# Kernel tuning notes

Measured on AMD Instinct MI355X. Metric: run time of the kernel, lower is better.

Reference implementation:

```python
import jax, jax.numpy as jnp
import numpy as np

N = 50000      # nodes
E = 1600000    # edges
H = 128        # node_hidden_size
T = 2          # num_prop_rounds


def setup_inputs() -> dict:
    key = jax.random.key(0)
    ks = jax.random.split(key, 10)
    s = 0.05
    return {
        "hv": jax.random.normal(ks[0], (N, H), dtype=jnp.float32),
        "edge_src": jax.random.randint(ks[1], (E,), 0, N, dtype=jnp.int64)
            if jax.config.jax_enable_x64 else jax.random.randint(ks[1], (E,), 0, N, dtype=jnp.int32),
        "edge_dst": jax.random.randint(ks[2], (E,), 0, N, dtype=jnp.int32),
        "msg_W": jax.random.normal(ks[3], (T, 2 * H, 2 * H), dtype=jnp.float32) * s,
        "msg_b": jax.random.normal(ks[4], (T, 2 * H), dtype=jnp.float32) * s,
        "gru_Wih": jax.random.normal(ks[5], (T, 3 * H, 2 * H), dtype=jnp.float32) * s,
        "gru_Whh": jax.random.normal(ks[6], (T, 3 * H, H), dtype=jnp.float32) * s,
        "gru_bih": jax.random.normal(ks[7], (T, 3 * H), dtype=jnp.float32) * s,
        "gru_bhh": jax.random.normal(ks[8], (T, 3 * H), dtype=jnp.float32) * s,
    }


def _gru_cell(a, h, Wih, Whh, bih, bhh):
    # PyTorch GRUCell gate order: reset, update, new
    gi = a @ Wih.T + bih           # [N, 3H]
    gh = h @ Whh.T + bhh           # [N, 3H]
    i_r, i_z, i_n = jnp.split(gi, 3, axis=-1)
    h_r, h_z, h_n = jnp.split(gh, 3, axis=-1)
    r = jax.nn.sigmoid(i_r + h_r)
    z = jax.nn.sigmoid(i_z + h_z)
    n = jnp.tanh(i_n + r * h_n)
    return (1.0 - z) * n + z * h


def reference(hv, edge_src, edge_dst, msg_W, msg_b, gru_Wih, gru_Whh, gru_bih, gru_bhh):
    n_nodes = hv.shape[0]
    for t in range(msg_W.shape[0]):
        # per-edge message: Linear(concat([h_dst, h_src]))  -> [E, 2H]
        h_src = hv[edge_src]
        h_dst = hv[edge_dst]
        msg = jnp.concatenate([h_dst, h_src], axis=-1) @ msg_W[t].T + msg_b[t]
        # mailbox sum per destination node -> activation a [N, 2H]
        a = jax.ops.segment_sum(msg, edge_dst, num_segments=n_nodes)
        # GRU update
        hv = _gru_cell(a, hv, gru_Wih[t], gru_Whh[t], gru_bih[t], gru_bhh[t])
    return hv
```

## Files before the change

kernel.cpp:

```cpp
#include <hip/hip_runtime.h>
#include <hip/hip_bf16.h>


#define NN 50000
#define NE 1600000
#define HH 128
#define TT 2
#define NB 1563
#define GG 64
#define EPB 25000
#define MAXB 3072

typedef _Float16 half8 __attribute__((ext_vector_type(8)));
typedef _Float16 half2v __attribute__((ext_vector_type(2)));
typedef float floatx4 __attribute__((ext_vector_type(4)));

__device__ __forceinline__ float bf2f(unsigned short u) {
    union { unsigned int i; float f; } c;
    c.i = ((unsigned int)u) << 16;
    return c.f;
}
__device__ __forceinline__ float ldf(const void* p, size_t i, int f32) {
    return f32 ? ((const float*)p)[i] : bf2f(((const unsigned short*)p)[i]);
}

__global__ void detect_kernel(const unsigned short* __restrict__ hv_u16,
                              const int* __restrict__ src, int* __restrict__ flags) {
    int i = threadIdx.x;
    int garbage = 0;
    for (int k = 0; k < 4; k++) {
        unsigned short u = hv_u16[2 * (i * 4 + k)];
        int e = (u >> 7) & 0xFF;
        if (e >= 0x90 || (e <= 0x60 && (u & 0x7FFF) != 0)) garbage++;
    }
    unsigned long long gb = __ballot(garbage > 0);
    int odd = src[2 * i + 1];
    unsigned long long bal = __ballot(odd == 0);
    if (i == 0) {
        flags[1] = (__popcll(gb) >= 8) ? 1 : 0;
        flags[0] = (bal == 0xFFFFFFFFFFFFFFFFull) ? 1 : 0;
    }
}

__global__ void split_kernel(const void* __restrict__ in, _Float16* __restrict__ ph,
                             _Float16* __restrict__ pl, int n, const int* __restrict__ flags) {
    int i = blockIdx.x * blockDim.x + threadIdx.x;
    if (i >= n) return;
    float v = ldf(in, i, flags[1]);
    _Float16 h = (_Float16)v;
    ph[i] = h;
    pl[i] = (_Float16)(v - (float)h);
}

__global__ void conv3_kernel(
    const void* __restrict__ i1, float* __restrict__ o1, int n1,
    const void* __restrict__ i2, float* __restrict__ o2, int n2,
    const void* __restrict__ i3, float* __restrict__ o3, int n3,
    const int* __restrict__ flags) {
    int i = blockIdx.x * blockDim.x + threadIdx.x;
    const void* in; float* out; int j = i;
    if (j < n1) { in = i1; out = o1; }
    else { j -= n1;
        if (j < n2) { in = i2; out = o2; }
        else { j -= n2; if (j >= n3) return; in = i3; out = o3; }
    }
    out[j] = ldf(in, j, flags[1]);
}

__global__ __launch_bounds__(256) void wc_kernel(
    const void* __restrict__ gWih, const void* __restrict__ msgW,
    _Float16* __restrict__ wcH, _Float16* __restrict__ wcL,
    const int* __restrict__ flags) {
    __shared__ float wrow[256];
    int tr = blockIdx.x;
    int t = tr / 384;
    int k = threadIdx.x;
    int f32 = flags[1];
    wrow[k] = ldf(gWih, (size_t)tr * 256 + k, f32);
    __syncthreads();
    float s = 0.f;
    size_t base = (size_t)t * 256 * 256;
    for (int c = 0; c < 256; c++)
        s += wrow[c] * ldf(msgW, base + (size_t)c * 256 + k, f32);
    _Float16 h = (_Float16)s;
    wcH[(size_t)tr * 256 + k] = h;
    wcL[(size_t)tr * 256 + k] = (_Float16)(s - (float)h);
}

__global__ void c1_kernel(const void* __restrict__ gWih, const float* __restrict__ bMsg,
                          float* __restrict__ c1, const int* __restrict__ flags) {
    int tr = blockIdx.x * 64 + threadIdx.x;
    if (tr >= TT * 384) return;
    int t = tr / 384;
    int f32 = flags[1];
    float s = 0.f;
    for (int c = 0; c < 256; c++)
        s += ldf(gWih, (size_t)tr * 256 + c, f32) * bMsg[t * 256 + c];
    c1[tr] = s;
}

__global__ __launch_bounds__(256) void bucket_hist_kernel(const int* __restrict__ dst,
                                                          int* __restrict__ counts ) {
    __shared__ int h[NB];
    int g = blockIdx.x, tid = threadIdx.x;
    for (int b = tid; b < NB; b += 256) h[b] = 0;
    __syncthreads();
    int beg = g * EPB, end = min(NE, beg + EPB);
    for (int e = beg + tid; e < end; e += 256) atomicAdd(&h[dst[e] >> 5], 1);
    __syncthreads();
    for (int b = tid; b < NB; b += 256) counts[b * GG + g] = h[b];
}

__global__ __launch_bounds__(256) void bucket_sum_kernel(const int* __restrict__ counts,
                                                         int* __restrict__ bsum) {
    int b = blockIdx.x * 4 + (threadIdx.x >> 6);
    int lane = threadIdx.x & 63;
    if (b >= NB) return;
    int v = counts[b * GG + lane];
    #pragma unroll
    for (int off = 32; off > 0; off >>= 1) v += __shfl_down(v, off, 64);
    if (lane == 0) bsum[b] = v;
}

__global__ void bucket_scan_kernel(const int* __restrict__ bsum, int* __restrict__ bbase) {
    __shared__ int wsum[16];
    __shared__ int s_running;
    int tid = threadIdx.x, lane = tid & 63, w = tid >> 6;
    if (tid == 0) s_running = 0;
    __syncthreads();
    int nch = (NB + 1024) / 1024;
    for (int c = 0; c < nch; c++) {
        int idx = c * 1024 + tid;
        int v = (idx < NB) ? bsum[idx] : 0;
        int s = v;
        #pragma unroll
        for (int off = 1; off < 64; off <<= 1) {
            int t = __shfl_up(s, off, 64);
            if (lane >= off) s += t;
        }
        if (lane == 63) wsum[w] = s;
        __syncthreads();
        if (w == 0) {
            int ws = (lane < 16) ? wsum[lane] : 0;
            #pragma unroll
            for (int off = 1; off < 16; off <<= 1) {
                int t = __shfl_up(ws, off, 64);
                if (lane >= off) ws += t;
            }
            if (lane < 16) wsum[lane] = ws;
        }
        __syncthreads();
        int incl = s + ((w > 0) ? wsum[w - 1] : 0);
        int base = s_running;
        if (idx <= NB) bbase[idx] = base + incl - v;
        __syncthreads();
        if (tid == 1023) s_running = base + incl;
        __syncthreads();
    }
}

__global__ __launch_bounds__(256) void bucket_offsets_kernel(const int* __restrict__ counts,
                                                             const int* __restrict__ bbase,
                                                             int* __restrict__ offsets) {
    int b = blockIdx.x * 4 + (threadIdx.x >> 6);
    int lane = threadIdx.x & 63;
    if (b >= NB) return;
    int v = counts[b * GG + lane];
    int s = v;
    #pragma unroll
    for (int off = 1; off < 64; off <<= 1) {
        int t = __shfl_up(s, off, 64);
        if (lane >= off) s += t;
    }
    offsets[b * GG + lane] = bbase[b] + s - v;
}

__global__ __launch_bounds__(256) void bucket_scatter_kernel(
    const int* __restrict__ src, const int* __restrict__ dst,
    const int* __restrict__ offsets, int* __restrict__ pairs,
    const int* __restrict__ flags) {
    __shared__ int ofs[NB];
    int g = blockIdx.x, tid = threadIdx.x;
    for (int b = tid; b < NB; b += 256) ofs[b] = offsets[b * GG + g];
    __syncthreads();
    int beg = g * EPB, end = min(NE, beg + EPB);
    int f64 = flags[0];
    for (int e = beg + tid; e < end; e += 256) {
        int d = dst[e];
        int s = f64 ? src[2 * e] : src[e];
        int pos = atomicAdd(&ofs[d >> 5], 1);
        pairs[pos] = ((d & 31) << 16) | s;
    }
}

__global__ __launch_bounds__(256) void bucket_sort_kernel(
    const int* __restrict__ bbase, int* __restrict__ pairs,
    int* __restrict__ row, int* __restrict__ deg) {
    __shared__ int buf[MAXB];
    __shared__ int cnt[32];
    __shared__ int off[32];
    int b = blockIdx.x, tid = threadIdx.x;
    int beg = bbase[b], end = bbase[b + 1];
    int nE = end - beg;
    if (nE > MAXB) nE = MAXB;
    if (tid < 32) cnt[tid] = 0;
    __syncthreads();
    for (int i = tid; i < nE; i += 256) {
        int pk = pairs[beg + i];
        buf[i] = pk;
        atomicAdd(&cnt[pk >> 16], 1);
    }
    __syncthreads();
    if (tid < 64) {
        int lane = tid;
        int v = (lane < 32) ? cnt[lane] : 0;
        int s = v;
        #pragma unroll
        for (int o = 1; o < 32; o <<= 1) {
            int t = __shfl_up(s, o, 64);
            if (lane >= o) s += t;
        }
        if (lane < 32) {
            off[lane] = s - v;
            int gn = b * 32 + lane;
            if (gn < NN) { row[gn] = beg + s - v; deg[gn] = v; }
        }
        if (lane == 0 && b == NB - 1) row[NN] = end;
    }
    __syncthreads();
    if (tid < 32) cnt[tid] = off[tid];
    __syncthreads();
    for (int i = tid; i < nE; i += 256) {
        int pk = buf[i];
        int pos = atomicAdd(&cnt[pk >> 16], 1);
        pairs[beg + pos] = pk & 0xFFFF;
    }
}

__global__ __launch_bounds__(64) void gather_kernel(
    const int* __restrict__ row, const int* __restrict__ csr,
    const _Float16* __restrict__ hvH,
    _Float16* __restrict__ SH, _Float16* __restrict__ SL) {
    int n = blockIdx.x;
    int lane = threadIdx.x;
    const half2v* hv2 = (const half2v*)hvH;
    int beg = row[n], end = row[n + 1];
    float sx = 0.f, sy = 0.f;
    int e = beg;
    for (; e + 8 <= end; e += 8) {
        int s0 = csr[e], s1 = csr[e + 1], s2 = csr[e + 2], s3 = csr[e + 3];
        int s4 = csr[e + 4], s5 = csr[e + 5], s6 = csr[e + 6], s7 = csr[e + 7];
        half2v v0 = hv2[(size_t)s0 * 64 + lane];
        half2v v1 = hv2[(size_t)s1 * 64 + lane];
        half2v v2 = hv2[(size_t)s2 * 64 + lane];
        half2v v3 = hv2[(size_t)s3 * 64 + lane];
        half2v v4 = hv2[(size_t)s4 * 64 + lane];
        half2v v5 = hv2[(size_t)s5 * 64 + lane];
        half2v v6 = hv2[(size_t)s6 * 64 + lane];
        half2v v7 = hv2[(size_t)s7 * 64 + lane];
        sx += (float)v0.x + (float)v1.x + (float)v2.x + (float)v3.x
            + (float)v4.x + (float)v5.x + (float)v6.x + (float)v7.x;
        sy += (float)v0.y + (float)v1.y + (float)v2.y + (float)v3.y
            + (float)v4.y + (float)v5.y + (float)v6.y + (float)v7.y;
    }
    for (; e < end; e++) {
        half2v v = hv2[(size_t)csr[e] * 64 + lane];
        sx += (float)v.x; sy += (float)v.y;
    }
    half2v hx, lx;
    hx.x = (_Float16)sx; lx.x = (_Float16)(sx - (float)hx.x);
    hx.y = (_Float16)sy; lx.y = (_Float16)(sy - (float)hx.y);
    ((half2v*)SH)[(size_t)n * 64 + lane] = hx;
    ((half2v*)SL)[(size_t)n * 64 + lane] = lx;
}

struct GemmOp {
    const _Float16 *AhA, *AlA, *AhB, *AlB;
    int Kleft, K;
    const _Float16 *Wh, *Wl;
    const float* bias;
    const float* bias2;
    _Float16* outH;
    int ldc, mode;
};

__global__ __launch_bounds__(256) void mfma_gemm_kernel(
    GemmOp op, const int* __restrict__ deg, int M) {
    __shared__ _Float16 Wsh[128][40];
    __shared__ _Float16 Wsl[128][40];
    int n0 = blockIdx.x * 128;
    int m0 = blockIdx.y * 128;
    int tid = threadIdx.x;
    int wave = tid >> 6, lane = tid & 63;
    int lr = lane & 15, quad = lane >> 4;
    int wm = wave * 32;
    floatx4 acc[2][8] = {};
    int r0 = tid >> 2, c0 = (tid & 3) * 8;

    float dsc[2] = {1.f, 1.f};
    if (op.mode == 0) {
        #pragma unroll
        for (int mt = 0; mt < 2; mt++) {
            int gm = m0 + wm + mt * 16 + lr;
            dsc[mt] = (gm < M) ? (float)deg[gm] : 0.f;
        }
    }

    for (int k0 = 0; k0 < op.K; k0 += 32) {
        half8 wh0 = *(const half8*)(op.Wh + (size_t)(n0 + r0) * op.K + k0 + c0);
        half8 wh1 = *(const half8*)(op.Wh + (size_t)(n0 + r0 + 64) * op.K + k0 + c0);
        half8 wl0 = *(const half8*)(op.Wl + (size_t)(n0 + r0) * op.K + k0 + c0);
        half8 wl1 = *(const half8*)(op.Wl + (size_t)(n0 + r0 + 64) * op.K + k0 + c0);
        bool left = (k0 < op.Kleft);
        const _Float16* Ph = left ? op.AhA : op.AhB;
        const _Float16* Pl = left ? op.AlA : op.AlB;
        int astr = left ? op.Kleft : (op.K - op.Kleft);
        int kk = (left ? k0 : k0 - op.Kleft) + quad * 8;
        half8 afh[2] = {}, afl[2] = {};
        #pragma unroll
        for (int mt = 0; mt < 2; mt++) {
            int gm = m0 + wm + mt * 16 + lr;
            if (gm < M) {
                afh[mt] = *(const half8*)(Ph + (size_t)gm * astr + kk);
                afl[mt] = *(const half8*)(Pl + (size_t)gm * astr + kk);
            }
        }
        if (op.mode == 0 && left) {
            #pragma unroll
            for (int mt = 0; mt < 2; mt++)
                #pragma unroll
                for (int q = 0; q < 8; q++) {
                    float f = ((float)afh[mt][q] + (float)afl[mt][q]) * dsc[mt];
                    _Float16 h = (_Float16)f;
                    afh[mt][q] = h; afl[mt][q] = (_Float16)(f - (float)h);
                }
        }
        __syncthreads();
        *(half8*)&Wsh[r0][c0] = wh0;   *(half8*)&Wsh[r0 + 64][c0] = wh1;
        *(half8*)&Wsl[r0][c0] = wl0;   *(half8*)&Wsl[r0 + 64][c0] = wl1;
        __syncthreads();
        #pragma unroll
        for (int nt = 0; nt < 8; nt++) {
            half8 bh = *(const half8*)&Wsh[nt * 16 + lr][quad * 8];
            half8 bl = *(const half8*)&Wsl[nt * 16 + lr][quad * 8];
            #pragma unroll
            for (int mt = 0; mt < 2; mt++) {
                acc[mt][nt] = __builtin_amdgcn_mfma_f32_16x16x32_f16(afh[mt], bh, acc[mt][nt], 0, 0, 0);
                acc[mt][nt] = __builtin_amdgcn_mfma_f32_16x16x32_f16(afl[mt], bh, acc[mt][nt], 0, 0, 0);
                acc[mt][nt] = __builtin_amdgcn_mfma_f32_16x16x32_f16(afh[mt], bl, acc[mt][nt], 0, 0, 0);
            }
        }
    }

    #pragma unroll
    for (int mt = 0; mt < 2; mt++) {
        #pragma unroll
        for (int r = 0; r < 4; r++) {
            int m = m0 + wm + mt * 16 + quad * 4 + r;
            if (m >= M) continue;
            float d2 = (op.mode == 0) ? (float)deg[m] : 0.f;
            #pragma unroll
            for (int nt = 0; nt < 8; nt++) {
                int n = n0 + nt * 16 + lr;
                float v = acc[mt][nt][r] + op.bias[n];
                if (op.mode == 0) v += d2 * op.bias2[n];
                op.outH[(size_t)m * op.ldc + n] = (_Float16)v;
            }
        }
    }
}

__global__ void gate_kernel(const _Float16* __restrict__ gi,
                            const _Float16* __restrict__ gh,
                            _Float16* __restrict__ hvH, _Float16* __restrict__ hvL,
                            void* __restrict__ outv,
                            const int* __restrict__ flags, int writeOut, int total) {
    int idx = blockIdx.x * blockDim.x + threadIdx.x;
    if (idx >= total) return;
    int n = idx >> 7;
    int j = idx & 127;
    size_t base = (size_t)n * 384;
    float i_r = (float)gi[base + j];
    float i_z = (float)gi[base + 128 + j];
    float i_n = (float)gi[base + 256 + j];
    float h_r = (float)gh[base + j];
    float h_z = (float)gh[base + 128 + j];
    float h_n = (float)gh[base + 256 + j];
    float h = (float)hvH[idx] + (float)hvL[idx];
    float r = 1.f / (1.f + __expf(-(i_r + h_r)));
    float z = 1.f / (1.f + __expf(-(i_z + h_z)));
    float nn = tanhf(i_n + r * h_n);
    float hn = (1.f - z) * nn + z * h;
    _Float16 hh = (_Float16)hn;
    hvH[idx] = hh;
    hvL[idx] = (_Float16)(hn - (float)hh);
    if (writeOut) {
        if (flags[1]) ((float*)outv)[idx] = hn;
        else ((__hip_bfloat16*)outv)[idx] = __float2bfloat16(hn);
    }
}

extern "C" void kernel_launch(void* const* d_in, const int* in_sizes, int n_in,
                              void* d_out, int out_size, void* d_ws, size_t ws_size,
                              hipStream_t stream) {
    const void* hv_in   = d_in[0];
    const int* edge_src = (const int*)d_in[1];
    const int* edge_dst = (const int*)d_in[2];
    const void* msg_W = d_in[3];
    const void* msg_b = d_in[4];
    const void* gWih  = d_in[5];
    const void* gWhh  = d_in[6];
    const void* gbih  = d_in[7];
    const void* gbhh  = d_in[8];

    char* p = (char*)d_ws;
    auto alloc = [&](size_t bytes) -> void* {
        void* r = (void*)p;
        p += (bytes + 255) & ~(size_t)255;
        return r;
    };
    int* flags   = (int*)alloc(256);
    int* deg     = (int*)alloc((size_t)NN * 4);
    int* row     = (int*)alloc((size_t)(NN + 1) * 4);
    int* counts  = (int*)alloc((size_t)NB * GG * 4);
    int* bsum    = (int*)alloc((size_t)NB * 4);
    int* bbase   = (int*)alloc((size_t)(NB + 1) * 4);
    int* offsets = (int*)alloc((size_t)NB * GG * 4);
    int* pairs   = (int*)alloc((size_t)NE * 4);
    _Float16* wCcH = (_Float16*)alloc((size_t)TT * 384 * 256 * 2);
    _Float16* wCcL = (_Float16*)alloc((size_t)TT * 384 * 256 * 2);
    _Float16* wHhH = (_Float16*)alloc((size_t)TT * 384 * 128 * 2);
    _Float16* wHhL = (_Float16*)alloc((size_t)TT * 384 * 128 * 2);
    float* bMsg = (float*)alloc((size_t)TT * 256 * 4);
    float* bIh  = (float*)alloc((size_t)TT * 384 * 4);
    float* bHh  = (float*)alloc((size_t)TT * 384 * 4);
    float* c1   = (float*)alloc((size_t)TT * 384 * 4);
    _Float16* hvH = (_Float16*)alloc((size_t)NN * HH * 2);
    _Float16* hvL = (_Float16*)alloc((size_t)NN * HH * 2);
    char* PA = (char*)alloc((size_t)NN * 384 * 2);
    char* PB = (char*)alloc((size_t)NN * 384 * 2);
    (void)ws_size; (void)in_sizes; (void)n_in; (void)out_size;

    _Float16* gi = (_Float16*)PA;
    _Float16* SH = (_Float16*)PB;
    _Float16* SL = (_Float16*)(PB + (size_t)NN * HH * 2);
    _Float16* gh = (_Float16*)PB;

    detect_kernel<<<1, 64, 0, stream>>>((const unsigned short*)hv_in, edge_src, flags);
    split_kernel<<<(NN * HH + 255) / 256, 256, 0, stream>>>(hv_in, hvH, hvL, NN * HH, flags);
    split_kernel<<<(TT * 384 * 128 + 255) / 256, 256, 0, stream>>>(
        gWhh, wHhH, wHhL, TT * 384 * 128, flags);
    {
        int n1 = TT * 256, n2 = TT * 384, n3 = TT * 384;
        conv3_kernel<<<(n1 + n2 + n3 + 255) / 256, 256, 0, stream>>>(
            msg_b, bMsg, n1, gbih, bIh, n2, gbhh, bHh, n3, flags);
    }
    wc_kernel<<<TT * 384, 256, 0, stream>>>(gWih, msg_W, wCcH, wCcL, flags);
    c1_kernel<<<(TT * 384 + 63) / 64, 64, 0, stream>>>(gWih, bMsg, c1, flags);

    bucket_hist_kernel<<<GG, 256, 0, stream>>>(edge_dst, counts);
    bucket_sum_kernel<<<(NB + 3) / 4, 256, 0, stream>>>(counts, bsum);
    bucket_scan_kernel<<<1, 1024, 0, stream>>>(bsum, bbase);
    bucket_offsets_kernel<<<(NB + 3) / 4, 256, 0, stream>>>(counts, bbase, offsets);
    bucket_scatter_kernel<<<GG, 256, 0, stream>>>(edge_src, edge_dst, offsets, pairs, flags);
    bucket_sort_kernel<<<NB, 256, 0, stream>>>(bbase, pairs, row, deg);

    int mt128 = (NN + 127) / 128;

    for (int t = 0; t < TT; t++) {
        gather_kernel<<<NN, 64, 0, stream>>>(row, pairs, hvH, SH, SL);

        GemmOp opi = { hvH, hvL, SH, SL, 128, 256,
                       wCcH + (size_t)t * 384 * 256, wCcL + (size_t)t * 384 * 256,
                       bIh + (size_t)t * 384, c1 + (size_t)t * 384, gi, 384, 0 };
        mfma_gemm_kernel<<<dim3(3, mt128), 256, 0, stream>>>(opi, deg, NN);

        GemmOp opg = { hvH, hvL, hvH, hvL, 128, 128,
                       wHhH + (size_t)t * 384 * 128, wHhL + (size_t)t * 384 * 128,
                       bHh + (size_t)t * 384, nullptr, gh, 384, 1 };
        mfma_gemm_kernel<<<dim3(3, mt128), 256, 0, stream>>>(opg, deg, NN);

        gate_kernel<<<(NN * HH + 255) / 256, 256, 0, stream>>>(
            gi, gh, hvH, hvL, d_out, flags, (t == TT - 1) ? 1 : 0, NN * HH);
    }
}
```

Measured before the change: 595.2 us.

## Fuse both GRU GEMMs and the gate into one per-round kernel

Replaces the two MFMA GEMM launches (input-side and hidden-side) and the separate gate kernel with a single fused kernel per round. Each 64-thread block handles 32 rows and 64 output columns, and computes the r, z and n gate chunks in turn, keeping r and z in shared memory. The last chunk applies the GRU update directly. This removes the global round-trip of the gi/gh intermediates (N x 384 fp16 each) and two launches, and double-buffers the hidden state so the kernel does not read rows it has already overwritten. In exchange, weights are now read straight from global memory with no shared-memory staging. The tiles are also small single-wave blocks, which may lower MFMA efficiency and increase weight traffic.

```diff
diff --git a/kernel.cpp b/kernel.cpp
--- a/kernel.cpp
+++ b/kernel.cpp
@@ -274,129 +274,140 @@
     ((half2v*)SL)[(size_t)n * 64 + lane] = lx;
 }
 
-struct GemmOp {
-    const _Float16 *AhA, *AlA, *AhB, *AlB;
-    int Kleft, K;
-    const _Float16 *Wh, *Wl;
-    const float* bias;
-    const float* bias2;
-    _Float16* outH;
-    int ldc, mode;
-};
-
-__global__ __launch_bounds__(256) void mfma_gemm_kernel(
-    GemmOp op, const int* __restrict__ deg, int M) {
-    __shared__ _Float16 Wsh[128][40];
-    __shared__ _Float16 Wsl[128][40];
-    int n0 = blockIdx.x * 128;
-    int m0 = blockIdx.y * 128;
-    int tid = threadIdx.x;
-    int wave = tid >> 6, lane = tid & 63;
-    int lr = lane & 15, quad = lane >> 4;
-    int wm = wave * 32;
-    floatx4 acc[2][8] = {};
-    int r0 = tid >> 2, c0 = (tid & 3) * 8;
-
-    float dsc[2] = {1.f, 1.f};
-    if (op.mode == 0) {
-        #pragma unroll
-        for (int mt = 0; mt < 2; mt++) {
-            int gm = m0 + wm + mt * 16 + lr;
-            dsc[mt] = (gm < M) ? (float)deg[gm] : 0.f;
-        }
-    }
-
-    for (int k0 = 0; k0 < op.K; k0 += 32) {
-        half8 wh0 = *(const half8*)(op.Wh + (size_t)(n0 + r0) * op.K + k0 + c0);
-        half8 wh1 = *(const half8*)(op.Wh + (size_t)(n0 + r0 + 64) * op.K + k0 + c0);
-        half8 wl0 = *(const half8*)(op.Wl + (size_t)(n0 + r0) * op.K + k0 + c0);
-        half8 wl1 = *(const half8*)(op.Wl + (size_t)(n0 + r0 + 64) * op.K + k0 + c0);
-        bool left = (k0 < op.Kleft);
-        const _Float16* Ph = left ? op.AhA : op.AhB;
-        const _Float16* Pl = left ? op.AlA : op.AlB;
-        int astr = left ? op.Kleft : (op.K - op.Kleft);
-        int kk = (left ? k0 : k0 - op.Kleft) + quad * 8;
-        half8 afh[2] = {}, afl[2] = {};
-        #pragma unroll
-        for (int mt = 0; mt < 2; mt++) {
-            int gm = m0 + wm + mt * 16 + lr;
-            if (gm < M) {
-                afh[mt] = *(const half8*)(Ph + (size_t)gm * astr + kk);
-                afl[mt] = *(const half8*)(Pl + (size_t)gm * astr + kk);
-            }
-        }
-        if (op.mode == 0 && left) {
+__global__ __launch_bounds__(64) void fused_round_kernel(
+    const _Float16* __restrict__ hvH, const _Float16* __restrict__ hvL,
+    const _Float16* __restrict__ SH, const _Float16* __restrict__ SL,
+    const _Float16* __restrict__ WcH, const _Float16* __restrict__ WcL,
+    const _Float16* __restrict__ WhH, const _Float16* __restrict__ WhL,
+    const float* __restrict__ bIh, const float* __restrict__ bHh,
+    const float* __restrict__ c1v, const int* __restrict__ deg,
+    _Float16* __restrict__ newH, _Float16* __restrict__ newL,
+    void* __restrict__ outv, const int* __restrict__ flags, int writeOut) {
+    __shared__ _Float16 rbuf[32][72];
+    __shared__ _Float16 zbuf[32][72];
+    const int cg = blockIdx.x;
+    const int m0 = blockIdx.y * 32;
+    const int lane = threadIdx.x;
+    const int lr = lane & 15, quad = lane >> 4;
+    const int kq = quad * 8;
+
+    int gmA[2]; bool vA[2];
+    #pragma unroll
+    for (int mt = 0; mt < 2; mt++) { gmA[mt] = m0 + mt * 16 + lr; vA[mt] = gmA[mt] < NN; }
+
+    float dmr[2][4];
+    #pragma unroll
+    for (int mt = 0; mt < 2; mt++)
+        #pragma unroll
+        for (int r = 0; r < 4; r++) {
+            int om = m0 + mt * 16 + quad * 4 + r;
+            dmr[mt][r] = (om < NN) ? (float)deg[om] : 0.f;
+        }
+
+    #pragma clang loop unroll(disable)
+    for (int c = 0; c < 3; c++) {
+        const int nb = c * 128 + cg * 64;
+        floatx4 accR[2][4], accL[2][4], accH[2][4];
+        #pragma unroll
+        for (int nt = 0; nt < 4; nt++) {
+            int n = nb + nt * 16 + lr;
+            float bi = bIh[n], cc = c1v[n], bg = bHh[n];
             #pragma unroll
             for (int mt = 0; mt < 2; mt++)
                 #pragma unroll
-                for (int q = 0; q < 8; q++) {
-                    float f = ((float)afh[mt][q] + (float)afl[mt][q]) * dsc[mt];
-                    _Float16 h = (_Float16)f;
-                    afh[mt][q] = h; afl[mt][q] = (_Float16)(f - (float)h);
+                for (int q = 0; q < 4; q++) {
+                    accR[mt][nt][q] = bi;
+                    accL[mt][nt][q] = cc;
+                    accH[mt][nt][q] = bg;
                 }
         }
-        __syncthreads();
-        *(half8*)&Wsh[r0][c0] = wh0;   *(half8*)&Wsh[r0 + 64][c0] = wh1;
-        *(half8*)&Wsl[r0][c0] = wl0;   *(half8*)&Wsl[r0 + 64][c0] = wl1;
-        __syncthreads();
-        #pragma unroll
-        for (int nt = 0; nt < 8; nt++) {
-            half8 bh = *(const half8*)&Wsh[nt * 16 + lr][quad * 8];
-            half8 bl = *(const half8*)&Wsl[nt * 16 + lr][quad * 8];
-            #pragma unroll
-            for (int mt = 0; mt < 2; mt++) {
-                acc[mt][nt] = __builtin_amdgcn_mfma_f32_16x16x32_f16(afh[mt], bh, acc[mt][nt], 0, 0, 0);
-                acc[mt][nt] = __builtin_amdgcn_mfma_f32_16x16x32_f16(afl[mt], bh, acc[mt][nt], 0, 0, 0);
-                acc[mt][nt] = __builtin_amdgcn_mfma_f32_16x16x32_f16(afh[mt], bl, acc[mt][nt], 0, 0, 0);
-            }
-        }
-    }
-
-    #pragma unroll
-    for (int mt = 0; mt < 2; mt++) {
-        #pragma unroll
-        for (int r = 0; r < 4; r++) {
-            int m = m0 + wm + mt * 16 + quad * 4 + r;
-            if (m >= M) continue;
-            float d2 = (op.mode == 0) ? (float)deg[m] : 0.f;
-            #pragma unroll
-            for (int nt = 0; nt < 8; nt++) {
-                int n = n0 + nt * 16 + lr;
-                float v = acc[mt][nt][r] + op.bias[n];
-                if (op.mode == 0) v += d2 * op.bias2[n];
-                op.outH[(size_t)m * op.ldc + n] = (_Float16)v;
-            }
-        }
-    }
-}
-
-__global__ void gate_kernel(const _Float16* __restrict__ gi,
-                            const _Float16* __restrict__ gh,
-                            _Float16* __restrict__ hvH, _Float16* __restrict__ hvL,
-                            void* __restrict__ outv,
-                            const int* __restrict__ flags, int writeOut, int total) {
-    int idx = blockIdx.x * blockDim.x + threadIdx.x;
-    if (idx >= total) return;
-    int n = idx >> 7;
-    int j = idx & 127;
-    size_t base = (size_t)n * 384;
-    float i_r = (float)gi[base + j];
-    float i_z = (float)gi[base + 128 + j];
-    float i_n = (float)gi[base + 256 + j];
-    float h_r = (float)gh[base + j];
-    float h_z = (float)gh[base + 128 + j];
-    float h_n = (float)gh[base + 256 + j];
-    float h = (float)hvH[idx] + (float)hvL[idx];
-    float r = 1.f / (1.f + __expf(-(i_r + h_r)));
-    float z = 1.f / (1.f + __expf(-(i_z + h_z)));
-    float nn = tanhf(i_n + r * h_n);
-    float hn = (1.f - z) * nn + z * h;
-    _Float16 hh = (_Float16)hn;
-    hvH[idx] = hh;
-    hvL[idx] = (_Float16)(hn - (float)hh);
-    if (writeOut) {
-        if (flags[1]) ((float*)outv)[idx] = hn;
-        else ((__hip_bfloat16*)outv)[idx] = __float2bfloat16(hn);
+        #pragma unroll
+        for (int k0 = 0; k0 < 128; k0 += 32) {
+            half8 afh[2] = {}, afl[2] = {};
+            #pragma unroll
+            for (int mt = 0; mt < 2; mt++) if (vA[mt]) {
+                afh[mt] = *(const half8*)(SH + (size_t)gmA[mt] * HH + k0 + kq);
+                afl[mt] = *(const half8*)(SL + (size_t)gmA[mt] * HH + k0 + kq);
+            }
+            #pragma unroll
+            for (int nt = 0; nt < 4; nt++) {
+                size_t wi = (size_t)(nb + nt * 16 + lr) * 256 + 128 + k0 + kq;
+                half8 bh = *(const half8*)(WcH + wi);
+                half8 bl = *(const half8*)(WcL + wi);
+                #pragma unroll
+                for (int mt = 0; mt < 2; mt++) {
+                    accR[mt][nt] = __builtin_amdgcn_mfma_f32_16x16x32_f16(afh[mt], bh, accR[mt][nt], 0, 0, 0);
+                    accR[mt][nt] = __builtin_amdgcn_mfma_f32_16x16x32_f16(afl[mt], bh, accR[mt][nt], 0, 0, 0);
+                    accR[mt][nt] = __builtin_amdgcn_mfma_f32_16x16x32_f16(afh[mt], bl, accR[mt][nt], 0, 0, 0);
+                }
+            }
+        }
+        #pragma unroll
+        for (int k0 = 0; k0 < 128; k0 += 32) {
+            half8 afh[2] = {}, afl[2] = {};
+            #pragma unroll
+            for (int mt = 0; mt < 2; mt++) if (vA[mt]) {
+                afh[mt] = *(const half8*)(hvH + (size_t)gmA[mt] * HH + k0 + kq);
+                afl[mt] = *(const half8*)(hvL + (size_t)gmA[mt] * HH + k0 + kq);
+            }
+            #pragma unroll
+            for (int nt = 0; nt < 4; nt++) {
+                size_t wi = (size_t)(nb + nt * 16 + lr) * 256 + k0 + kq;
+                half8 bh = *(const half8*)(WcH + wi);
+                half8 bl = *(const half8*)(WcL + wi);
+                #pragma unroll
+                for (int mt = 0; mt < 2; mt++) {
+                    accL[mt][nt] = __builtin_amdgcn_mfma_f32_16x16x32_f16(afh[mt], bh, accL[mt][nt], 0, 0, 0);
+                    accL[mt][nt] = __builtin_amdgcn_mfma_f32_16x16x32_f16(afl[mt], bh, accL[mt][nt], 0, 0, 0);
+                    accL[mt][nt] = __builtin_amdgcn_mfma_f32_16x16x32_f16(afh[mt], bl, accL[mt][nt], 0, 0, 0);
+                }
+            }
+            #pragma unroll
+            for (int nt = 0; nt < 4; nt++) {
+                size_t wi = (size_t)(nb + nt * 16 + lr) * HH + k0 + kq;
+                half8 bh = *(const half8*)(WhH + wi);
+                half8 bl = *(const half8*)(WhL + wi);
+                #pragma unroll
+                for (int mt = 0; mt < 2; mt++) {
+                    accH[mt][nt] = __builtin_amdgcn_mfma_f32_16x16x32_f16(afh[mt], bh, accH[mt][nt], 0, 0, 0);
+                    accH[mt][nt] = __builtin_amdgcn_mfma_f32_16x16x32_f16(afl[mt], bh, accH[mt][nt], 0, 0, 0);
+                    accH[mt][nt] = __builtin_amdgcn_mfma_f32_16x16x32_f16(afh[mt], bl, accH[mt][nt], 0, 0, 0);
+                }
+            }
+        }
+        #pragma unroll
+        for (int mt = 0; mt < 2; mt++)
+            #pragma unroll
+            for (int nt = 0; nt < 4; nt++)
+                #pragma unroll
+                for (int r = 0; r < 4; r++) {
+                    int lrow = mt * 16 + quad * 4 + r;
+                    int lcol = nt * 16 + lr;
+                    float gi = dmr[mt][r] * accL[mt][nt][r] + accR[mt][nt][r];
+                    float gh = accH[mt][nt][r];
+                    if (c == 0) {
+                        rbuf[lrow][lcol] = (_Float16)(1.f / (1.f + __expf(-(gi + gh))));
+                    } else if (c == 1) {
+                        zbuf[lrow][lcol] = (_Float16)(1.f / (1.f + __expf(-(gi + gh))));
+                    } else {
+                        int om = m0 + lrow;
+                        if (om < NN) {
+                            float rv = (float)rbuf[lrow][lcol];
+                            float zv = (float)zbuf[lrow][lcol];
+                            float nv = tanhf(gi + rv * gh);
+                            size_t hidx = (size_t)om * HH + cg * 64 + lcol;
+                            float h = (float)hvH[hidx] + (float)hvL[hidx];
+                            float hn = (1.f - zv) * nv + zv * h;
+                            _Float16 hh = (_Float16)hn;
+                            newH[hidx] = hh;
+                            newL[hidx] = (_Float16)(hn - (float)hh);
+                            if (writeOut) {
+                                if (flags[1]) ((float*)outv)[hidx] = hn;
+                                else ((__hip_bfloat16*)outv)[hidx] = __float2bfloat16(hn);
+                            }
+                        }
+                    }
+                }
     }
 }
 
@@ -435,19 +446,16 @@
     float* bIh  = (float*)alloc((size_t)TT * 384 * 4);
     float* bHh  = (float*)alloc((size_t)TT * 384 * 4);
     float* c1   = (float*)alloc((size_t)TT * 384 * 4);
-    _Float16* hvH = (_Float16*)alloc((size_t)NN * HH * 2);
-    _Float16* hvL = (_Float16*)alloc((size_t)NN * HH * 2);
-    char* PA = (char*)alloc((size_t)NN * 384 * 2);
-    char* PB = (char*)alloc((size_t)NN * 384 * 2);
+    _Float16* hvAH = (_Float16*)alloc((size_t)NN * HH * 2);
+    _Float16* hvAL = (_Float16*)alloc((size_t)NN * HH * 2);
+    _Float16* hvBH = (_Float16*)alloc((size_t)NN * HH * 2);
+    _Float16* hvBL = (_Float16*)alloc((size_t)NN * HH * 2);
+    _Float16* SH   = (_Float16*)alloc((size_t)NN * HH * 2);
+    _Float16* SL   = (_Float16*)alloc((size_t)NN * HH * 2);
     (void)ws_size; (void)in_sizes; (void)n_in; (void)out_size;
 
-    _Float16* gi = (_Float16*)PA;
-    _Float16* SH = (_Float16*)PB;
-    _Float16* SL = (_Float16*)(PB + (size_t)NN * HH * 2);
-    _Float16* gh = (_Float16*)PB;
-
     detect_kernel<<<1, 64, 0, stream>>>((const unsigned short*)hv_in, edge_src, flags);
-    split_kernel<<<(NN * HH + 255) / 256, 256, 0, stream>>>(hv_in, hvH, hvL, NN * HH, flags);
+    split_kernel<<<(NN * HH + 255) / 256, 256, 0, stream>>>(hv_in, hvAH, hvAL, NN * HH, flags);
     split_kernel<<<(TT * 384 * 128 + 255) / 256, 256, 0, stream>>>(
         gWhh, wHhH, wHhL, TT * 384 * 128, flags);
     {
@@ -465,22 +473,21 @@
     bucket_scatter_kernel<<<GG, 256, 0, stream>>>(edge_src, edge_dst, offsets, pairs, flags);
     bucket_sort_kernel<<<NB, 256, 0, stream>>>(bbase, pairs, row, deg);
 
-    int mt128 = (NN + 127) / 128;
+    const int mt32 = (NN + 31) / 32;
+    _Float16 *cH = hvAH, *cL = hvAL, *nH = hvBH, *nL = hvBL;
 
     for (int t = 0; t < TT; t++) {
-        gather_kernel<<<NN, 64, 0, stream>>>(row, pairs, hvH, SH, SL);
-
-        GemmOp opi = { hvH, hvL, SH, SL, 128, 256,
-                       wCcH + (size_t)t * 384 * 256, wCcL + (size_t)t * 384 * 256,
-                       bIh + (size_t)t * 384, c1 + (size_t)t * 384, gi, 384, 0 };
-        mfma_gemm_kernel<<<dim3(3, mt128), 256, 0, stream>>>(opi, deg, NN);
-
-        GemmOp opg = { hvH, hvL, hvH, hvL, 128, 128,
-                       wHhH + (size_t)t * 384 * 128, wHhL + (size_t)t * 384 * 128,
-                       bHh + (size_t)t * 384, nullptr, gh, 384, 1 };
-        mfma_gemm_kernel<<<dim3(3, mt128), 256, 0, stream>>>(opg, deg, NN);
-
-        gate_kernel<<<(NN * HH + 255) / 256, 256, 0, stream>>>(
-            gi, gh, hvH, hvL, d_out, flags, (t == TT - 1) ? 1 : 0, NN * HH);
-    }
-}
+        gather_kernel<<<NN, 64, 0, stream>>>(row, pairs, cH, SH, SL);
+
+        fused_round_kernel<<<dim3(2, mt32), 64, 0, stream>>>(
+            cH, cL, SH, SL,
+            wCcH + (size_t)t * 384 * 256, wCcL + (size_t)t * 384 * 256,
+            wHhH + (size_t)t * 384 * 128, wHhL + (size_t)t * 384 * 128,
+            bIh + (size_t)t * 384, bHh + (size_t)t * 384, c1 + (size_t)t * 384,
+            deg, nH, nL, d_out, flags, (t == TT - 1) ? 1 : 0);
+
+        _Float16* sw;
+        sw = cH; cH = nH; nH = sw;
+        sw = cL; cL = nL; nL = sw;
+    }
+}
```

Measured after the change: 838.6 us. 40.9% more time.

## Template GEMM with whole-K weight tile in LDS, XCD-aware block remap

Applied to the files above, without the earlier changes.

Replaces the runtime-parameterized GEMM with a templated kernel that loads the full-K weight slice for a 64-column tile into shared memory once, so the K loop no longer has per-step barriers. The degree scaling of the hv-part is moved out of the per-element split/recombine and applied in the epilogue through a separate left accumulator. Block IDs are remapped so neighbouring tiles land on the same XCD, and the grid becomes 1D with 64-wide N tiles. In exchange it doubles A-matrix reloads across N tiles and uses more LDS per block.

```diff
diff --git a/kernel.cpp b/kernel.cpp
--- a/kernel.cpp
+++ b/kernel.cpp
@@ -274,80 +274,93 @@
     ((half2v*)SL)[(size_t)n * 64 + lane] = lx;
 }
 
-struct GemmOp {
-    const _Float16 *AhA, *AlA, *AhB, *AlB;
-    int Kleft, K;
-    const _Float16 *Wh, *Wl;
-    const float* bias;
-    const float* bias2;
-    _Float16* outH;
-    int ldc, mode;
-};
-
-__global__ __launch_bounds__(256) void mfma_gemm_kernel(
-    GemmOp op, const int* __restrict__ deg, int M) {
-    __shared__ _Float16 Wsh[128][40];
-    __shared__ _Float16 Wsl[128][40];
-    int n0 = blockIdx.x * 128;
-    int m0 = blockIdx.y * 128;
+template<int KK, int KLEFT, int MODE>
+__global__ __launch_bounds__(256) void gemm_t(
+    const _Float16* __restrict__ AhA, const _Float16* __restrict__ AlA,
+    const _Float16* __restrict__ AhB, const _Float16* __restrict__ AlB,
+    const _Float16* __restrict__ Wh,  const _Float16* __restrict__ Wl,
+    const float* __restrict__ bias, const float* __restrict__ bias2,
+    _Float16* __restrict__ outC, const int* __restrict__ deg, int M) {
+    constexpr int LDW = KK + 8;
+    __shared__ _Float16 Wsh[64][LDW];
+    __shared__ _Float16 Wsl[64][LDW];
+
+    int nwg = gridDim.x;
+    int q = nwg >> 3, r = nwg & 7;
+    int xcd = blockIdx.x & 7, pos = blockIdx.x >> 3;
+    int wid = (xcd < r ? xcd * (q + 1) : r * (q + 1) + (xcd - r) * q) + pos;
+    int n0 = (wid % 6) * 64;
+    int m0 = (wid / 6) * 128;
+
     int tid = threadIdx.x;
     int wave = tid >> 6, lane = tid & 63;
     int lr = lane & 15, quad = lane >> 4;
     int wm = wave * 32;
-    floatx4 acc[2][8] = {};
-    int r0 = tid >> 2, c0 = (tid & 3) * 8;
-
-    float dsc[2] = {1.f, 1.f};
-    if (op.mode == 0) {
-        #pragma unroll
-        for (int mt = 0; mt < 2; mt++) {
-            int gm = m0 + wm + mt * 16 + lr;
-            dsc[mt] = (gm < M) ? (float)deg[gm] : 0.f;
-        }
-    }
-
-    for (int k0 = 0; k0 < op.K; k0 += 32) {
-        half8 wh0 = *(const half8*)(op.Wh + (size_t)(n0 + r0) * op.K + k0 + c0);
-        half8 wh1 = *(const half8*)(op.Wh + (size_t)(n0 + r0 + 64) * op.K + k0 + c0);
-        half8 wl0 = *(const half8*)(op.Wl + (size_t)(n0 + r0) * op.K + k0 + c0);
-        half8 wl1 = *(const half8*)(op.Wl + (size_t)(n0 + r0 + 64) * op.K + k0 + c0);
-        bool left = (k0 < op.Kleft);
-        const _Float16* Ph = left ? op.AhA : op.AhB;
-        const _Float16* Pl = left ? op.AlA : op.AlB;
-        int astr = left ? op.Kleft : (op.K - op.Kleft);
-        int kk = (left ? k0 : k0 - op.Kleft) + quad * 8;
+
+    {
+        constexpr int TPR = KK / 8;
+        constexpr int RPP = 256 / TPR;
+        int rr = tid / TPR;
+        int cc = (tid % TPR) * 8;
+        #pragma unroll
+        for (int base = 0; base < 64; base += RPP) {
+            *(half8*)&Wsh[base + rr][cc] =
+                *(const half8*)(Wh + (size_t)(n0 + base + rr) * KK + cc);
+            *(half8*)&Wsl[base + rr][cc] =
+                *(const half8*)(Wl + (size_t)(n0 + base + rr) * KK + cc);
+        }
+    }
+    __syncthreads();
+
+    int gm[2]; bool vm[2];
+    #pragma unroll
+    for (int mt = 0; mt < 2; mt++) { gm[mt] = m0 + wm + mt * 16 + lr; vm[mt] = gm[mt] < M; }
+
+    floatx4 accL[2][4] = {};
+    floatx4 accR[2][4] = {};
+
+    if (MODE == 0) {
+        #pragma unroll
+        for (int k0 = 0; k0 < KLEFT; k0 += 32) {
+            int kk = k0 + quad * 8;
+            half8 afh[2] = {}, afl[2] = {};
+            #pragma unroll
+            for (int mt = 0; mt < 2; mt++) if (vm[mt]) {
+                afh[mt] = *(const half8*)(AhA + (size_t)gm[mt] * HH + kk);
+                afl[mt] = *(const half8*)(AlA + (size_t)gm[mt] * HH + kk);
+            }
+            #pragma unroll
+            for (int nt = 0; nt < 4; nt++) {
+                half8 bh = *(const half8*)&Wsh[nt * 16 + lr][kk];
+                half8 bl = *(const half8*)&Wsl[nt * 16 + lr][kk];
+                #pragma unroll
+                for (int mt = 0; mt < 2; mt++) {
+                    accL[mt][nt] = __builtin_amdgcn_mfma_f32_16x16x32_f16(afh[mt], bh, accL[mt][nt], 0, 0, 0);
+                    accL[mt][nt] = __builtin_amdgcn_mfma_f32_16x16x32_f16(afl[mt], bh, accL[mt][nt], 0, 0, 0);
+                    accL[mt][nt] = __builtin_amdgcn_mfma_f32_16x16x32_f16(afh[mt], bl, accL[mt][nt], 0, 0, 0);
+                }
+            }
+        }
+    }
+    #pragma unroll
+    for (int k0 = KLEFT; k0 < KK; k0 += 32) {
+        int kk = k0 + quad * 8;
+        int kr = (k0 - KLEFT) + quad * 8;
         half8 afh[2] = {}, afl[2] = {};
         #pragma unroll
-        for (int mt = 0; mt < 2; mt++) {
-            int gm = m0 + wm + mt * 16 + lr;
-            if (gm < M) {
-                afh[mt] = *(const half8*)(Ph + (size_t)gm * astr + kk);
-                afl[mt] = *(const half8*)(Pl + (size_t)gm * astr + kk);
-            }
-        }
-        if (op.mode == 0 && left) {
-            #pragma unroll
-            for (int mt = 0; mt < 2; mt++)
-                #pragma unroll
-                for (int q = 0; q < 8; q++) {
-                    float f = ((float)afh[mt][q] + (float)afl[mt][q]) * dsc[mt];
-                    _Float16 h = (_Float16)f;
-                    afh[mt][q] = h; afl[mt][q] = (_Float16)(f - (float)h);
-                }
-        }
-        __syncthreads();
-        *(half8*)&Wsh[r0][c0] = wh0;   *(half8*)&Wsh[r0 + 64][c0] = wh1;
-        *(half8*)&Wsl[r0][c0] = wl0;   *(half8*)&Wsl[r0 + 64][c0] = wl1;
-        __syncthreads();
-        #pragma unroll
-        for (int nt = 0; nt < 8; nt++) {
-            half8 bh = *(const half8*)&Wsh[nt * 16 + lr][quad * 8];
-            half8 bl = *(const half8*)&Wsl[nt * 16 + lr][quad * 8];
+        for (int mt = 0; mt < 2; mt++) if (vm[mt]) {
+            afh[mt] = *(const half8*)(AhB + (size_t)gm[mt] * HH + kr);
+            afl[mt] = *(const half8*)(AlB + (size_t)gm[mt] * HH + kr);
+        }
+        #pragma unroll
+        for (int nt = 0; nt < 4; nt++) {
+            half8 bh = *(const half8*)&Wsh[nt * 16 + lr][kk];
+            half8 bl = *(const half8*)&Wsl[nt * 16 + lr][kk];
             #pragma unroll
             for (int mt = 0; mt < 2; mt++) {
-                acc[mt][nt] = __builtin_amdgcn_mfma_f32_16x16x32_f16(afh[mt], bh, acc[mt][nt], 0, 0, 0);
-                acc[mt][nt] = __builtin_amdgcn_mfma_f32_16x16x32_f16(afl[mt], bh, acc[mt][nt], 0, 0, 0);
-                acc[mt][nt] = __builtin_amdgcn_mfma_f32_16x16x32_f16(afh[mt], bl, acc[mt][nt], 0, 0, 0);
+                accR[mt][nt] = __builtin_amdgcn_mfma_f32_16x16x32_f16(afh[mt], bh, accR[mt][nt], 0, 0, 0);
+                accR[mt][nt] = __builtin_amdgcn_mfma_f32_16x16x32_f16(afl[mt], bh, accR[mt][nt], 0, 0, 0);
+                accR[mt][nt] = __builtin_amdgcn_mfma_f32_16x16x32_f16(afh[mt], bl, accR[mt][nt], 0, 0, 0);
             }
         }
     }
@@ -355,16 +368,16 @@
     #pragma unroll
     for (int mt = 0; mt < 2; mt++) {
         #pragma unroll
-        for (int r = 0; r < 4; r++) {
-            int m = m0 + wm + mt * 16 + quad * 4 + r;
+        for (int rr2 = 0; rr2 < 4; rr2++) {
+            int m = m0 + wm + mt * 16 + quad * 4 + rr2;
             if (m >= M) continue;
-            float d2 = (op.mode == 0) ? (float)deg[m] : 0.f;
+            float dv = (MODE == 0) ? (float)deg[m] : 0.f;
             #pragma unroll
-            for (int nt = 0; nt < 8; nt++) {
+            for (int nt = 0; nt < 4; nt++) {
                 int n = n0 + nt * 16 + lr;
-                float v = acc[mt][nt][r] + op.bias[n];
-                if (op.mode == 0) v += d2 * op.bias2[n];
-                op.outH[(size_t)m * op.ldc + n] = (_Float16)v;
+                float v = accR[mt][nt][rr2] + bias[n];
+                if (MODE == 0) v += dv * (accL[mt][nt][rr2] + bias2[n]);
+                outC[(size_t)m * 384 + n] = (_Float16)v;
             }
         }
     }
@@ -465,20 +478,21 @@
     bucket_scatter_kernel<<<GG, 256, 0, stream>>>(edge_src, edge_dst, offsets, pairs, flags);
     bucket_sort_kernel<<<NB, 256, 0, stream>>>(bbase, pairs, row, deg);
 
-    int mt128 = (NN + 127) / 128;
+    const int mt128 = (NN + 127) / 128;
+    const int nblk = mt128 * 6;
 
     for (int t = 0; t < TT; t++) {
         gather_kernel<<<NN, 64, 0, stream>>>(row, pairs, hvH, SH, SL);
 
-        GemmOp opi = { hvH, hvL, SH, SL, 128, 256,
-                       wCcH + (size_t)t * 384 * 256, wCcL + (size_t)t * 384 * 256,
-                       bIh + (size_t)t * 384, c1 + (size_t)t * 384, gi, 384, 0 };
-        mfma_gemm_kernel<<<dim3(3, mt128), 256, 0, stream>>>(opi, deg, NN);
-
-        GemmOp opg = { hvH, hvL, hvH, hvL, 128, 128,
-                       wHhH + (size_t)t * 384 * 128, wHhL + (size_t)t * 384 * 128,
-                       bHh + (size_t)t * 384, nullptr, gh, 384, 1 };
-        mfma_gemm_kernel<<<dim3(3, mt128), 256, 0, stream>>>(opg, deg, NN);
+        gemm_t<256, 128, 0><<<nblk, 256, 0, stream>>>(
+            hvH, hvL, SH, SL,
+            wCcH + (size_t)t * 384 * 256, wCcL + (size_t)t * 384 * 256,
+            bIh + (size_t)t * 384, c1 + (size_t)t * 384, gi, deg, NN);
+
+        gemm_t<128, 0, 1><<<nblk, 256, 0, stream>>>(
+            hvH, hvL, hvH, hvL,
+            wHhH + (size_t)t * 384 * 128, wHhL + (size_t)t * 384 * 128,
+            bHh + (size_t)t * 384, nullptr, gh, deg, NN);
 
         gate_kernel<<<(NN * HH + 255) / 256, 256, 0, stream>>>(
             gi, gh, hvH, hvL, d_out, flags, (t == TT - 1) ? 1 : 0, NN * HH);
```

Result: faster. 561.3 us (-5.7%).
